# Performance work log

Hardware: AMD Instinct MI355X
Metric: run time of the kernel (lower is better)

The kernel has to match this reference:

```python
import jax, jax.numpy as jnp
import numpy as np

D_FIELDS = 16
HIDDEN = 16
N_POINTS = 1_000_000


def setup_inputs() -> dict:
    key = jax.random.key(0)
    ks = jax.random.split(key, 7)
    x = jax.random.normal(ks[0], (1, 3, N_POINTS), dtype=jnp.float32)
    # stacked per-field Conv1d(k=1) weights: conv weight [out,in,1] -> matrix [out,in]
    W1 = jax.random.normal(ks[1], (D_FIELDS, HIDDEN, 3), dtype=jnp.float32) * 0.1
    b1 = jax.random.normal(ks[2], (D_FIELDS, HIDDEN), dtype=jnp.float32) * 0.1
    W2 = jax.random.normal(ks[3], (D_FIELDS, HIDDEN, HIDDEN), dtype=jnp.float32) * 0.1
    b2 = jax.random.normal(ks[4], (D_FIELDS, HIDDEN), dtype=jnp.float32) * 0.1
    W3 = jax.random.normal(ks[5], (D_FIELDS, 3, HIDDEN), dtype=jnp.float32) * 0.1
    b3 = jax.random.normal(ks[6], (D_FIELDS, 3), dtype=jnp.float32) * 0.1
    return {"x": x, "W1": W1, "b1": b1, "W2": W2, "b2": b2, "W3": W3, "b3": b3, "D": D_FIELDS}


def reference(x, W1, b1, W2, b2, W3, b3, D):
    # x: [1, 3, N]. Original loops d in range(D) applying field d's MLP to x and
    # concatenating along dim 0 -> [D, 3, N]. Fused here as batched GEMMs over d.
    xs = x[0]  # [3, N]
    h = jax.nn.relu(jnp.einsum('dhc,cn->dhn', W1, xs) + b1[:, :, None])      # [D,H,N]
    h = jax.nn.relu(jnp.einsum('dgh,dhn->dgn', W2, h) + b2[:, :, None])      # [D,H,N]
    out = jnp.einsum('doh,dhn->don', W3, h) + b3[:, :, None]                 # [D,3,N]
    return out
```

## Files before the change

kernel.cpp:

```cpp
#include <hip/hip_runtime.h>


#define MFMA16(a, b, c) __builtin_amdgcn_mfma_f32_16x16x16f16((a), (b), (c), 0, 0, 0)

#define TILES_PER_WAVE 25
#define WAVES_PER_BLOCK 4
#define FPB 4
#define PTS_PER_WAVE (TILES_PER_WAVE * 16)
#define PTS_PER_BLOCK (PTS_PER_WAVE * WAVES_PER_BLOCK)

typedef __fp16 pk16x2 __attribute__((ext_vector_type(2)));
typedef _Float16 half4_t __attribute__((ext_vector_type(4)));
typedef float float4_t __attribute__((ext_vector_type(4)));

union H2I { pk16x2 h; int i; };
union Frag { half4_t v; int i[2]; };

__device__ __forceinline__ int pkrtz(float a, float b) {
    H2I u; u.h = __builtin_amdgcn_cvt_pkrtz(a, b); return u.i;
}

__device__ __forceinline__ int pk_relu_pack(float a, float b) {
    H2I u; u.h = __builtin_amdgcn_cvt_pkrtz(a, b);
    const pk16x2 z = {(__fp16)0.f, (__fp16)0.f};
    u.h = __builtin_elementwise_max(u.h, z);
    return u.i;
}

__global__ __launch_bounds__(256) void fields_r11_kernel(
    const float* __restrict__ x,
    const float* __restrict__ W1, const float* __restrict__ b1,
    const float* __restrict__ W2, const float* __restrict__ b2,
    const float* __restrict__ W3, const float* __restrict__ b3,
    float* __restrict__ out, int N)
{
    const int lane = threadIdx.x & 63;
    const int wave = threadIdx.x >> 6;
    const int q    = lane >> 4;
    const int n16  = lane & 15;

    const int bid = blockIdx.x;
    const int r   = bid & 7;
    const int dg  = (bid >> 3) & 3;
    const int a   = bid >> 5;
    const int chunk  = a * 8 + r;
    const int chunks = (N + PTS_PER_BLOCK - 1) / PTS_PER_BLOCK;
    if (chunk >= chunks) return;

    const int base = chunk * PTS_PER_BLOCK + wave * PTS_PER_WAVE;
    const bool isq0 = (q == 0);

    Frag a1w[FPB], a2w[FPB], a3w[FPB];
    float4_t b1v[FPB], b2v[FPB], b3v[FPB];
#pragma unroll
    for (int f = 0; f < FPB; ++f) {
        const int d = dg * FPB + f;
        const float* w1 = W1 + (d * 16 + n16) * 3;
        a1w[f].v = (half4_t){(_Float16)w1[0], (_Float16)w1[1],
                             (_Float16)w1[2], (_Float16)0.f};
        const float4_t w2 = *(const float4_t*)(W2 + (d * 16 + n16) * 16 + q * 4);
        a2w[f].v = (half4_t){(_Float16)w2.x, (_Float16)w2.y, (_Float16)w2.z,
                             (_Float16)w2.w};
        if (n16 < 3) {
            const float4_t w3 = *(const float4_t*)(W3 + (d * 3 + n16) * 16 + q * 4);
            a3w[f].v = (half4_t){(_Float16)w3.x, (_Float16)w3.y, (_Float16)w3.z,
                                 (_Float16)w3.w};
        } else {
            a3w[f].i[0] = 0; a3w[f].i[1] = 0;
        }
        b1v[f] = *(const float4_t*)(b1 + d * 16 + q * 4);
        b2v[f] = *(const float4_t*)(b2 + d * 16 + q * 4);
        float4_t bb3 = (float4_t){0.f, 0.f, 0.f, 0.f};
        if (isq0) {
            bb3.x = b3[d * 3 + 0];
            bb3.y = b3[d * 3 + 1];
            bb3.z = b3[d * 3 + 2];
        }
        b3v[f] = bb3;
    }

    const float* xb0 = x + base;
    const float* xb1 = xb0 + N;
    const float* xb2 = xb1 + N;
    float* ob[FPB][3];
#pragma unroll
    for (int f = 0; f < FPB; ++f) {
        const int d = dg * FPB + f;
#pragma unroll
        for (int i = 0; i < 3; ++i)
            ob[f][i] = out + (size_t)(d * 3 + i) * N + base;
    }

    if (base + PTS_PER_WAVE <= N) {
        float c0 = xb0[n16], c1 = xb1[n16], c2 = xb2[n16];
#pragma unroll
        for (int t = 0; t < TILES_PER_WAVE; ++t) {
            const int off = t * 16;
            float nx0 = 0.f, nx1 = 0.f, nx2 = 0.f;
            if (t + 1 < TILES_PER_WAVE) {
                nx0 = xb0[n16 + off + 16];
                nx1 = xb1[n16 + off + 16];
                nx2 = xb2[n16 + off + 16];
            }
            const int p01 = pkrtz(c0, c1);
            const int p2  = pkrtz(c2, 0.f);
            Frag xf;
            xf.i[0] = isq0 ? p01 : 0;
            xf.i[1] = isq0 ? p2  : 0;

            float4_t acc[FPB];
#pragma unroll
            for (int f = 0; f < FPB; ++f) acc[f] = MFMA16(a1w[f].v, xf.v, b1v[f]);
            Frag hf[FPB];
#pragma unroll
            for (int f = 0; f < FPB; ++f) {
                hf[f].i[0] = pk_relu_pack(acc[f].x, acc[f].y);
                hf[f].i[1] = pk_relu_pack(acc[f].z, acc[f].w);
            }
#pragma unroll
            for (int f = 0; f < FPB; ++f) acc[f] = MFMA16(a2w[f].v, hf[f].v, b2v[f]);
#pragma unroll
            for (int f = 0; f < FPB; ++f) {
                hf[f].i[0] = pk_relu_pack(acc[f].x, acc[f].y);
                hf[f].i[1] = pk_relu_pack(acc[f].z, acc[f].w);
            }
#pragma unroll
            for (int f = 0; f < FPB; ++f) acc[f] = MFMA16(a3w[f].v, hf[f].v, b3v[f]);
            if (isq0) {
#pragma unroll
                for (int f = 0; f < FPB; ++f) {
                    ob[f][0][n16 + off] = acc[f].x;
                    ob[f][1][n16 + off] = acc[f].y;
                    ob[f][2][n16 + off] = acc[f].z;
                }
            }
            c0 = nx0; c1 = nx1; c2 = nx2;
        }
    } else {
#pragma unroll 1
        for (int t = 0; t < TILES_PER_WAVE; ++t) {
            const int off = t * 16;
            const int pt = base + off + n16;
            float x0 = 0.f, x1v = 0.f, x2v = 0.f;
            if (isq0 && pt < N) {
                x0  = xb0[n16 + off];
                x1v = xb1[n16 + off];
                x2v = xb2[n16 + off];
            }
            Frag xf;
            xf.i[0] = pkrtz(x0, x1v);
            xf.i[1] = pkrtz(x2v, 0.f);
#pragma unroll
            for (int f = 0; f < FPB; ++f) {
                float4_t acc = MFMA16(a1w[f].v, xf.v, b1v[f]);
                Frag bf;
                bf.i[0] = pk_relu_pack(acc.x, acc.y);
                bf.i[1] = pk_relu_pack(acc.z, acc.w);
                acc = MFMA16(a2w[f].v, bf.v, b2v[f]);
                Frag cf;
                cf.i[0] = pk_relu_pack(acc.x, acc.y);
                cf.i[1] = pk_relu_pack(acc.z, acc.w);
                acc = MFMA16(a3w[f].v, cf.v, b3v[f]);
                if (isq0 && pt < N) {
                    ob[f][0][n16 + off] = acc.x;
                    ob[f][1][n16 + off] = acc.y;
                    ob[f][2][n16 + off] = acc.z;
                }
            }
        }
    }
}

extern "C" void kernel_launch(void* const* d_in, const int* in_sizes, int n_in,
                              void* d_out, int out_size, void* d_ws, size_t ws_size,
                              hipStream_t stream) {
    const float* x  = (const float*)d_in[0];
    const float* W1 = (const float*)d_in[1];
    const float* b1 = (const float*)d_in[2];
    const float* W2 = (const float*)d_in[3];
    const float* b2 = (const float*)d_in[4];
    const float* W3 = (const float*)d_in[5];
    const float* b3 = (const float*)d_in[6];
    float* out = (float*)d_out;

    const int N = in_sizes[0] / 3;
    const int chunks = (N + PTS_PER_BLOCK - 1) / PTS_PER_BLOCK;
    const int a_max  = (chunks + 7) / 8;
    const int grid   = 8 * 4 * a_max;
    fields_r11_kernel<<<grid, 256, 0, stream>>>(x, W1, b1, W2, b2, W3, b3, out, N);
}
```

Baseline: 276.1 us.

## Halve fields per block and batch tiles in double-buffered groups

Each block now handles 2 fields instead of 4, so the grid doubles to 8 field groups. Within a wave, tiles are processed in groups of 5 with double-buffered x prefetch, and the MFMA chain is interleaved across tiles instead of across fields. A launch-bounds occupancy hint is added. The aim is more independent MFMAs in flight and better latency hiding, at the cost of reading x twice as often and possibly using more registers.

Result: faster. 250.7 us (-9.2%).

```diff
diff --git a/kernel.cpp b/kernel.cpp
--- a/kernel.cpp
+++ b/kernel.cpp
@@ -3,9 +3,11 @@
 
 #define MFMA16(a, b, c) __builtin_amdgcn_mfma_f32_16x16x16f16((a), (b), (c), 0, 0, 0)
 
-#define TILES_PER_WAVE 25
+#define GP 5
+#define NG 5
+#define TILES_PER_WAVE (GP * NG)
 #define WAVES_PER_BLOCK 4
-#define FPB 4
+#define FPB 2
 #define PTS_PER_WAVE (TILES_PER_WAVE * 16)
 #define PTS_PER_BLOCK (PTS_PER_WAVE * WAVES_PER_BLOCK)
 
@@ -27,7 +29,7 @@
     return u.i;
 }
 
-__global__ __launch_bounds__(256) void fields_r11_kernel(
+__global__ __launch_bounds__(256, 4) void fields_r12_kernel(
     const float* __restrict__ x,
     const float* __restrict__ W1, const float* __restrict__ b1,
     const float* __restrict__ W2, const float* __restrict__ b2,
@@ -41,8 +43,8 @@
 
     const int bid = blockIdx.x;
     const int r   = bid & 7;
-    const int dg  = (bid >> 3) & 3;
-    const int a   = bid >> 5;
+    const int fg  = (bid >> 3) & 7;
+    const int a   = bid >> 6;
     const int chunk  = a * 8 + r;
     const int chunks = (N + PTS_PER_BLOCK - 1) / PTS_PER_BLOCK;
     if (chunk >= chunks) return;
@@ -54,7 +56,7 @@
     float4_t b1v[FPB], b2v[FPB], b3v[FPB];
 #pragma unroll
     for (int f = 0; f < FPB; ++f) {
-        const int d = dg * FPB + f;
+        const int d = fg * FPB + f;
         const float* w1 = W1 + (d * 16 + n16) * 3;
         a1w[f].v = (half4_t){(_Float16)w1[0], (_Float16)w1[1],
                              (_Float16)w1[2], (_Float16)0.f};
@@ -85,56 +87,74 @@
     float* ob[FPB][3];
 #pragma unroll
     for (int f = 0; f < FPB; ++f) {
-        const int d = dg * FPB + f;
+        const int d = fg * FPB + f;
 #pragma unroll
         for (int i = 0; i < 3; ++i)
             ob[f][i] = out + (size_t)(d * 3 + i) * N + base;
     }
 
     if (base + PTS_PER_WAVE <= N) {
-        float c0 = xb0[n16], c1 = xb1[n16], c2 = xb2[n16];
-#pragma unroll
-        for (int t = 0; t < TILES_PER_WAVE; ++t) {
-            const int off = t * 16;
-            float nx0 = 0.f, nx1 = 0.f, nx2 = 0.f;
-            if (t + 1 < TILES_PER_WAVE) {
-                nx0 = xb0[n16 + off + 16];
-                nx1 = xb1[n16 + off + 16];
-                nx2 = xb2[n16 + off + 16];
-            }
-            const int p01 = pkrtz(c0, c1);
-            const int p2  = pkrtz(c2, 0.f);
-            Frag xf;
-            xf.i[0] = isq0 ? p01 : 0;
-            xf.i[1] = isq0 ? p2  : 0;
-
-            float4_t acc[FPB];
-#pragma unroll
-            for (int f = 0; f < FPB; ++f) acc[f] = MFMA16(a1w[f].v, xf.v, b1v[f]);
-            Frag hf[FPB];
+        float xb[2][3][GP];
+#pragma unroll
+        for (int t = 0; t < GP; ++t) {
+            xb[0][0][t] = xb0[n16 + t * 16];
+            xb[0][1][t] = xb1[n16 + t * 16];
+            xb[0][2][t] = xb2[n16 + t * 16];
+        }
+#pragma unroll
+        for (int g = 0; g < NG; ++g) {
+            const int b = g & 1;
+            if (g + 1 < NG) {
+                const int nb = (g + 1) & 1;
+#pragma unroll
+                for (int t = 0; t < GP; ++t) {
+                    const int off = n16 + ((g + 1) * GP + t) * 16;
+                    xb[nb][0][t] = xb0[off];
+                    xb[nb][1][t] = xb1[off];
+                    xb[nb][2][t] = xb2[off];
+                }
+            }
+            Frag xf[GP];
+#pragma unroll
+            for (int t = 0; t < GP; ++t) {
+                const int p01 = pkrtz(xb[b][0][t], xb[b][1][t]);
+                const int p2  = pkrtz(xb[b][2][t], 0.f);
+                xf[t].i[0] = isq0 ? p01 : 0;
+                xf[t].i[1] = isq0 ? p2  : 0;
+            }
 #pragma unroll
             for (int f = 0; f < FPB; ++f) {
-                hf[f].i[0] = pk_relu_pack(acc[f].x, acc[f].y);
-                hf[f].i[1] = pk_relu_pack(acc[f].z, acc[f].w);
-            }
-#pragma unroll
-            for (int f = 0; f < FPB; ++f) acc[f] = MFMA16(a2w[f].v, hf[f].v, b2v[f]);
-#pragma unroll
-            for (int f = 0; f < FPB; ++f) {
-                hf[f].i[0] = pk_relu_pack(acc[f].x, acc[f].y);
-                hf[f].i[1] = pk_relu_pack(acc[f].z, acc[f].w);
-            }
-#pragma unroll
-            for (int f = 0; f < FPB; ++f) acc[f] = MFMA16(a3w[f].v, hf[f].v, b3v[f]);
-            if (isq0) {
-#pragma unroll
-                for (int f = 0; f < FPB; ++f) {
-                    ob[f][0][n16 + off] = acc[f].x;
-                    ob[f][1][n16 + off] = acc[f].y;
-                    ob[f][2][n16 + off] = acc[f].z;
-                }
-            }
-            c0 = nx0; c1 = nx1; c2 = nx2;
+                float4_t acc[GP];
+#pragma unroll
+                for (int t = 0; t < GP; ++t)
+                    acc[t] = MFMA16(a1w[f].v, xf[t].v, b1v[f]);
+                Frag hf[GP];
+#pragma unroll
+                for (int t = 0; t < GP; ++t) {
+                    hf[t].i[0] = pk_relu_pack(acc[t].x, acc[t].y);
+                    hf[t].i[1] = pk_relu_pack(acc[t].z, acc[t].w);
+                }
+#pragma unroll
+                for (int t = 0; t < GP; ++t)
+                    acc[t] = MFMA16(a2w[f].v, hf[t].v, b2v[f]);
+#pragma unroll
+                for (int t = 0; t < GP; ++t) {
+                    hf[t].i[0] = pk_relu_pack(acc[t].x, acc[t].y);
+                    hf[t].i[1] = pk_relu_pack(acc[t].z, acc[t].w);
+                }
+#pragma unroll
+                for (int t = 0; t < GP; ++t)
+                    acc[t] = MFMA16(a3w[f].v, hf[t].v, b3v[f]);
+                if (isq0) {
+#pragma unroll
+                    for (int t = 0; t < GP; ++t) {
+                        const int off = n16 + (g * GP + t) * 16;
+                        ob[f][0][off] = acc[t].x;
+                        ob[f][1][off] = acc[t].y;
+                        ob[f][2][off] = acc[t].z;
+                    }
+                }
+            }
         }
     } else {
 #pragma unroll 1
@@ -186,6 +206,6 @@
     const int N = in_sizes[0] / 3;
     const int chunks = (N + PTS_PER_BLOCK - 1) / PTS_PER_BLOCK;
     const int a_max  = (chunks + 7) / 8;
-    const int grid   = 8 * 4 * a_max;
-    fields_r11_kernel<<<grid, 256, 0, stream>>>(x, W1, b1, W2, b2, W3, b3, out, N);
-}
+    const int grid   = 8 * 8 * a_max;
+    fields_r12_kernel<<<grid, 256, 0, stream>>>(x, W1, b1, W2, b2, W3, b3, out, N);
+}
```
